# Kernel optimization log

Measured on AMD Instinct MI355X. Metric: run time of the kernel, lower is better.

## Reference

```python
import jax, jax.numpy as jnp
import numpy as np

DIM = 1024
H = 16
DH = DIM // H  # 64


def _l2norm(a):
    # matches torch F.normalize(dim=-1, eps=1e-12)
    n = jnp.linalg.norm(a, axis=-1, keepdims=True)
    return a / jnp.maximum(n, 1e-12)


def setup_inputs() -> dict:
    key = jax.random.key(0)
    ks = jax.random.split(key, 6)
    B, T = 4, 4096
    s = 0.02
    return {
        "x": jax.random.normal(ks[0], (B, T, DIM), jnp.float32),
        "Wqkv": jax.random.normal(ks[1], (3 * DIM, DIM), jnp.float32) * s,
        "Wg": jax.random.normal(ks[2], (H, DIM), jnp.float32) * s,
        "bg": jnp.zeros((H,), jnp.float32),
        "Wb": jax.random.normal(ks[3], (H, DIM), jnp.float32) * s,
        "bb": jnp.zeros((H,), jnp.float32),
        "Wout": jax.random.normal(ks[4], (DIM, DIM), jnp.float32) * s,
    }


def reference(x, Wqkv, Wg, bg, Wb, bb, Wout):
    B, T, D = x.shape
    qkv = (x @ Wqkv.T).reshape(B, T, 3, H, DH)
    q = _l2norm(qkv[:, :, 0])   # [B,T,H,Dh]
    k = _l2norm(qkv[:, :, 1])
    v = qkv[:, :, 2]
    alpha = jax.nn.sigmoid(x @ Wg.T + bg)  # [B,T,H]
    beta = jax.nn.sigmoid(x @ Wb.T + bb)   # [B,T,H]

    # time-major for scan
    qT = jnp.moveaxis(q, 1, 0)  # [T,B,H,Dh]
    kT = jnp.moveaxis(k, 1, 0)
    vT = jnp.moveaxis(v, 1, 0)
    aT = jnp.moveaxis(alpha, 1, 0)  # [T,B,H]
    bT = jnp.moveaxis(beta, 1, 0)

    S0 = jnp.zeros((B, H, DH, DH), jnp.float32)

    def step(S, inp):
        q_t, k_t, v_t, a_t, b_t = inp
        Sk = jnp.einsum('bhij,bhj->bhi', S, k_t)          # S @ k_t
        a = a_t[..., None, None]
        b = b_t[..., None, None]
        # S = a * (S - b * (S k) k^T) + b * v k^T
        S = a * (S - b * Sk[..., :, None] * k_t[..., None, :]) \
            + b * v_t[..., :, None] * k_t[..., None, :]
        o = jnp.einsum('bhij,bhj->bhi', S, q_t)
        return S, o

    _, outs = jax.lax.scan(step, S0, (qT, kT, vT, aT, bT))  # [T,B,H,Dh]
    out = jnp.moveaxis(outs, 0, 1).reshape(B, T, D)
    return out @ Wout.T
```

## Files before the change

### kernel.cpp

```cpp
#include <hip/hip_runtime.h>
#include <hip/hip_bf16.h>

#define NB   4
#define NT   4096
#define BT   16384
#define NDIM 1024
#define NH   16
#define NDH  64
#define CC   64
#define NCH  (NT / CC)
#define NPAIR 64
#define NU   (NPAIR * NCH)
#define DBS  24

using u16 = unsigned short;
typedef __bf16 bf16x8 __attribute__((ext_vector_type(8)));
typedef float f32x4 __attribute__((ext_vector_type(4)));
typedef unsigned short u16x8 __attribute__((ext_vector_type(8)));
typedef unsigned short u16x4 __attribute__((ext_vector_type(4)));

__device__ __forceinline__ float bf2f(u16 b) { return __uint_as_float(((unsigned)b) << 16); }
__device__ __forceinline__ u16 f2bf(float f) {
  return __builtin_bit_cast(u16, __float2bfloat16(f));
}
__device__ __forceinline__ int swz(int row, int e) { return e ^ ((row & 7) << 3); }
__device__ __forceinline__ bf16x8 zfrag() {
  u16x8 z = {0, 0, 0, 0, 0, 0, 0, 0};
  return __builtin_bit_cast(bf16x8, z);
}
__device__ __forceinline__ long qkvT_idx(int s, int h, long bt, int d) {
  return ((long)(s * 16 + h) * BT + bt) * 64 + d;
}

__global__ __launch_bounds__(256) void k_f32_to_bf16(const float* __restrict__ in,
                                                     u16* __restrict__ out, long n4) {
  long i = (long)blockIdx.x * blockDim.x + threadIdx.x;
  if (i >= n4) return;
  float4 f = reinterpret_cast<const float4*>(in)[i];
  u16x4 o;
  o.x = f2bf(f.x); o.y = f2bf(f.y); o.z = f2bf(f.z); o.w = f2bf(f.w);
  reinterpret_cast<u16x4*>(out)[i] = o;
}

__global__ __launch_bounds__(256) void k_build_wgb(const float* __restrict__ Wg,
                                                   const float* __restrict__ Wb,
                                                   u16* __restrict__ out) {
  int i = blockIdx.x * 256 + threadIdx.x;
  int row = i >> 10, col = i & 1023;
  float f = 0.f;
  if (row < 16)       f = Wg[row * 1024 + col];
  else if (row < 32)  f = Wb[(row - 16) * 1024 + col];
  out[i] = f2bf(f);
}

typedef unsigned int u32_as1 __attribute__((address_space(1)));
typedef unsigned int u32_as3 __attribute__((address_space(3)));
__device__ __forceinline__ void gload_lds16(const void* g, void* l) {
  __builtin_amdgcn_global_load_lds((const u32_as1*)g, (u32_as3*)l, 16, 0, 0);
}

template <typename OutT>
__global__ __launch_bounds__(256) void k_gemm_bt(const u16* __restrict__ A,
                                                 const u16* __restrict__ B,
                                                 OutT* __restrict__ C,
                                                 int M, int N, int K) {
  constexpr int BM = 128, BN = 128, BK = 32;
  __shared__ __align__(16) u16 As[BM * BK];
  __shared__ __align__(16) u16 Bs[BN * BK];
  const int tid = threadIdx.x;
  const int l = tid & 63, w = tid >> 6;
  const int tn = blockIdx.x, tm = blockIdx.y;
  const long a0 = (long)tm * BM * K;
  const long b0 = (long)tn * BN * K;
  const int srow = tid >> 2;
  const int scol = (tid & 3) << 3;
  const int wrow = (w >> 1) << 6;
  const int wcol = (w & 1) << 6;
  const int fr = l & 15, fq = l >> 4;

  f32x4 acc[4][4];
#pragma unroll
  for (int m = 0; m < 4; ++m)
#pragma unroll
    for (int n = 0; n < 4; ++n) acc[m][n] = f32x4{0.f, 0.f, 0.f, 0.f};

  for (int kk = 0; kk < K; kk += BK) {
    __syncthreads();
    const u16* gA = A + a0 + (long)srow * K + kk + scol;
    const u16* gB = B + b0 + (long)srow * K + kk + scol;
    gload_lds16(gA,                &As[(w * 16) * BK]);
    gload_lds16(gA + 64 * (long)K, &As[(64 + w * 16) * BK]);
    gload_lds16(gB,                &Bs[(w * 16) * BK]);
    gload_lds16(gB + 64 * (long)K, &Bs[(64 + w * 16) * BK]);
    __syncthreads();

    bf16x8 af[4], bfv[4];
#pragma unroll
    for (int m = 0; m < 4; ++m)
      af[m] = *(const bf16x8*)&As[(wrow + m * 16 + fr) * BK + (fq << 3)];
#pragma unroll
    for (int n = 0; n < 4; ++n)
      bfv[n] = *(const bf16x8*)&Bs[(wcol + n * 16 + fr) * BK + (fq << 3)];
#pragma unroll
    for (int m = 0; m < 4; ++m)
#pragma unroll
      for (int n = 0; n < 4; ++n)
        acc[m][n] = __builtin_amdgcn_mfma_f32_16x16x32_bf16(af[m], bfv[n], acc[m][n], 0, 0, 0);
  }

#pragma unroll
  for (int m = 0; m < 4; ++m) {
#pragma unroll
    for (int n = 0; n < 4; ++n) {
      const int r0 = tm * BM + wrow + m * 16 + fq * 4;
      const int c  = tn * BN + wcol + n * 16 + fr;
#pragma unroll
      for (int r = 0; r < 4; ++r) {
        float v = acc[m][n][r];
        long idx = (long)(r0 + r) * N + c;
        if constexpr (sizeof(OutT) == 2) C[idx] = f2bf(v);
        else                             C[idx] = v;
      }
    }
  }
}

template <typename OutT, bool QKVT>
__global__ __launch_bounds__(512, 2) void k_gemm256(const u16* __restrict__ A,
                                                    const u16* __restrict__ B,
                                                    OutT* __restrict__ C,
                                                    int M, int N, int K) {
  __shared__ __align__(16) u16 As[2][2][256 * 32];
  __shared__ __align__(16) u16 Bs[2][2][256 * 32];
  const int tid = threadIdx.x;
  const int l = tid & 63, w = tid >> 6;
  const int wm = w >> 2, wn = w & 3;
  const int fr = l & 15, fq = l >> 4;
  const int nwg = gridDim.x;
  const int cpx = nwg >> 3;
  const int bid = blockIdx.x;
  const int sbid = (bid & 7) * cpx + (bid >> 3);
  const int ntn = N >> 8;
  const int tm = sbid / ntn, tn = sbid - tm * ntn;
  const long a0 = (long)tm * 256 * K;
  const long b0 = (long)tn * 256 * K;
  const int srow0 = tid >> 2;
  const int scol8 = (((tid & 3) ^ ((tid >> 4) & 3)) << 3);
  const int cswz = ((fq ^ ((fr >> 2) & 3)) << 3);
  const int NKT = K >> 6;

  auto stage_half = [&](int kt, int buf, int hf) {
    const int ks = hf >> 1;
    const u16* Gp = (hf & 1) ? B : A;
    const long g0 = ((hf & 1) ? b0 : a0) + (long)kt * 64 + ks * 32 + scol8;
    u16* lb = (hf & 1) ? &Bs[buf][ks][w * 512] : &As[buf][ks][w * 512];
#pragma unroll
    for (int r = 0; r < 2; ++r)
      gload_lds16(Gp + g0 + (long)(r * 128 + srow0) * K, lb + r * 4096);
  };

  f32x4 acc[8][4];
#pragma unroll
  for (int m = 0; m < 8; ++m)
#pragma unroll
    for (int n = 0; n < 4; ++n) acc[m][n] = f32x4{0.f, 0.f, 0.f, 0.f};

  stage_half(0, 0, 0); stage_half(0, 0, 1); stage_half(0, 0, 2); stage_half(0, 0, 3);

  for (int kt = 0; kt < NKT; ++kt) {
    const int bi = kt & 1;
    const bool pf = (kt + 1 < NKT);
    asm volatile("s_waitcnt vmcnt(4)" ::: "memory");
    __builtin_amdgcn_sched_barrier(0);
    __builtin_amdgcn_s_barrier();
    __builtin_amdgcn_sched_barrier(0);
    {
      const u16* ap = &As[bi][0][(wm * 128 + fr) * 32 + cswz];
      const u16* bp = &Bs[bi][0][(wn * 64 + fr) * 32 + cswz];
      bf16x8 bfr[4], afr[4];
#pragma unroll
      for (int n = 0; n < 4; ++n) bfr[n] = *(const bf16x8*)(bp + n * 512);
#pragma unroll
      for (int m = 0; m < 4; ++m) afr[m] = *(const bf16x8*)(ap + m * 512);
      if (pf) stage_half(kt + 1, bi ^ 1, 0);
      __builtin_amdgcn_s_setprio(1);
#pragma unroll
      for (int m = 0; m < 4; ++m)
#pragma unroll
        for (int n = 0; n < 4; ++n)
          acc[m][n] = __builtin_amdgcn_mfma_f32_16x16x32_bf16(afr[m], bfr[n], acc[m][n], 0, 0, 0);
      __builtin_amdgcn_s_setprio(0);
#pragma unroll
      for (int m = 0; m < 4; ++m) afr[m] = *(const bf16x8*)(ap + (4 + m) * 512);
      if (pf) stage_half(kt + 1, bi ^ 1, 1);
      __builtin_amdgcn_s_setprio(1);
#pragma unroll
      for (int m = 0; m < 4; ++m)
#pragma unroll
        for (int n = 0; n < 4; ++n)
          acc[4 + m][n] = __builtin_amdgcn_mfma_f32_16x16x32_bf16(afr[m], bfr[n], acc[4 + m][n], 0, 0, 0);
      __builtin_amdgcn_s_setprio(0);
    }
    if (pf) { asm volatile("s_waitcnt vmcnt(4)" ::: "memory"); }
    else    { asm volatile("s_waitcnt vmcnt(0)" ::: "memory"); }
    __builtin_amdgcn_sched_barrier(0);
    __builtin_amdgcn_s_barrier();
    __builtin_amdgcn_sched_barrier(0);
    {
      const u16* ap = &As[bi][1][(wm * 128 + fr) * 32 + cswz];
      const u16* bp = &Bs[bi][1][(wn * 64 + fr) * 32 + cswz];
      bf16x8 bfr[4], afr[4];
#pragma unroll
      for (int n = 0; n < 4; ++n) bfr[n] = *(const bf16x8*)(bp + n * 512);
#pragma unroll
      for (int m = 0; m < 4; ++m) afr[m] = *(const bf16x8*)(ap + m * 512);
      if (pf) stage_half(kt + 1, bi ^ 1, 2);
      __builtin_amdgcn_s_setprio(1);
#pragma unroll
      for (int m = 0; m < 4; ++m)
#pragma unroll
        for (int n = 0; n < 4; ++n)
          acc[m][n] = __builtin_amdgcn_mfma_f32_16x16x32_bf16(afr[m], bfr[n], acc[m][n], 0, 0, 0);
      __builtin_amdgcn_s_setprio(0);
#pragma unroll
      for (int m = 0; m < 4; ++m) afr[m] = *(const bf16x8*)(ap + (4 + m) * 512);
      if (pf) stage_half(kt + 1, bi ^ 1, 3);
      __builtin_amdgcn_s_setprio(1);
#pragma unroll
      for (int m = 0; m < 4; ++m)
#pragma unroll
        for (int n = 0; n < 4; ++n)
          acc[4 + m][n] = __builtin_amdgcn_mfma_f32_16x16x32_bf16(afr[m], bfr[n], acc[4 + m][n], 0, 0, 0);
      __builtin_amdgcn_s_setprio(0);
    }
  }

#pragma unroll
  for (int m = 0; m < 8; ++m)
#pragma unroll
    for (int n = 0; n < 4; ++n) {
      const int row0 = tm * 256 + wm * 128 + m * 16 + fq * 4;
      const int col  = tn * 256 + wn * 64 + n * 16 + fr;
#pragma unroll
      for (int r = 0; r < 4; ++r) {
        if constexpr (QKVT) {
          const int hb = (tn * 256 + wn * 64) >> 6;
          long idx = ((long)hb * BT + (row0 + r)) * 64 + (n * 16 + fr);
          C[idx] = (OutT)f2bf(acc[m][n][r]);
        } else {
          long idx = (long)(row0 + r) * N + col;
          if constexpr (sizeof(OutT) == 2) C[idx] = f2bf(acc[m][n][r]);
          else                             C[idx] = acc[m][n][r];
        }
      }
    }
}

__global__ __launch_bounds__(256) void k_gates_fin(const float* __restrict__ raw,
                                                   const float* __restrict__ bg,
                                                   const float* __restrict__ bb,
                                                   float* __restrict__ alpha,
                                                   float* __restrict__ beta) {
  int i = blockIdx.x * 256 + threadIdx.x;
  if (i >= BT * NH) return;
  int bt = i >> 4, h = i & 15;
  float ga = raw[(long)bt * 128 + h] + bg[h];
  float gb = raw[(long)bt * 128 + 16 + h] + bb[h];
  alpha[i] = 1.f / (1.f + __expf(-ga));
  beta[i]  = 1.f / (1.f + __expf(-gb));
}

__global__ __launch_bounds__(256, 3) void k_prep(u16* __restrict__ qkv,
                                                 const float* __restrict__ alpha,
                                                 const float* __restrict__ beta,
                                                 float* __restrict__ A63G,
                                                 u16* __restrict__ oi) {
  __shared__ __align__(16) u16 Ks[64 * 64];
  __shared__ __align__(16) u16 WTs[128 * 64];
  __shared__ __align__(16) u16 Lb[64 * 64];
  __shared__ __align__(16) u16 MqS[64 * 64];
  __shared__ __align__(16) u16 KdT[64 * 64];
  __shared__ __align__(16) u16 Db[4 * 16 * DBS];
  __shared__ float cvec[64], Avec[64], bvec[64], nkinv[64], nqinv[64];

  const int unit = blockIdx.x;
  const int pair = unit >> 6, ch = unit & 63;
  const int b = pair >> 4, h = pair & 15;
  const int tid = threadIdx.x, l = tid & 63, w = tid >> 6;
  const int fr = l & 15, fq = l >> 4;
  const long t0 = (long)b * NT + (long)ch * CC;

  u16x8 kreg[2], vreg[2], qreg[2];
  int srow_[2], sseg_[2];
#pragma unroll
  for (int p = 0; p < 2; ++p) {
    int idx = p * 256 + tid;
    srow_[p] = idx >> 3; sseg_[p] = (idx & 7) * 8;
    qreg[p] = *(const u16x8*)&qkv[qkvT_idx(0, h, t0 + srow_[p], sseg_[p])];
    kreg[p] = *(const u16x8*)&qkv[qkvT_idx(1, h, t0 + srow_[p], sseg_[p])];
    vreg[p] = *(const u16x8*)&qkv[qkvT_idx(2, h, t0 + srow_[p], sseg_[p])];
  }
  const int ar = w * 16 + fr;
  u16x8 qa[2];
#pragma unroll
  for (int kk = 0; kk < 2; ++kk)
    qa[kk] = *(const u16x8*)&qkv[qkvT_idx(0, h, t0 + ar, kk * 32 + fq * 8)];

  if (w == 0) {
    float av = alpha[(t0 + l) * 16 + h];
    float bv = beta[(t0 + l) * 16 + h];
    float cl = __log2f(av);
#pragma unroll
    for (int d = 1; d < 64; d <<= 1) {
      float up = __shfl_up(cl, d);
      if (l >= d) cl += up;
    }
    float A = exp2f(cl);
    cvec[l] = cl; Avec[l] = A; bvec[l] = bv;
    if (l == 63) A63G[unit] = A;
  }
  __syncthreads();

#pragma unroll
  for (int p = 0; p < 2; ++p) {
    int row = srow_[p], seg = sseg_[p];
    *(u16x8*)&Ks[row * 64 + swz(row, seg)] = kreg[p];
    float kss = 0.f, qss = 0.f;
    const float bs = bvec[row];
#pragma unroll
    for (int e = 0; e < 8; ++e) {
      float kf = bf2f(kreg[p][e]), qf = bf2f(qreg[p][e]);
      kss += kf * kf; qss += qf * qf;
      int c = seg + e;
      WTs[c * 64 + swz(c, row)] = f2bf(bs * bf2f(vreg[p][e]));
    }
    kss += __shfl_xor(kss, 1); kss += __shfl_xor(kss, 2); kss += __shfl_xor(kss, 4);
    qss += __shfl_xor(qss, 1); qss += __shfl_xor(qss, 2); qss += __shfl_xor(qss, 4);
    if ((tid & 7) == 0) { nkinv[row] = kss; nqinv[row] = qss; }
  }
  __syncthreads();

  if (tid < 64)       nkinv[tid] = rsqrtf(fmaxf(nkinv[tid], 1e-24f));
  else if (tid < 128) nqinv[tid - 64] = rsqrtf(fmaxf(nqinv[tid - 64], 1e-24f));
  __syncthreads();

  f32x4 akk[4], aqk[4];
#pragma unroll
  for (int n = 0; n < 4; ++n) { akk[n] = f32x4{0, 0, 0, 0}; aqk[n] = f32x4{0, 0, 0, 0}; }
  {
    bf16x8 afK[2], afQ[2];
#pragma unroll
    for (int kk = 0; kk < 2; ++kk) {
      afK[kk] = __builtin_bit_cast(bf16x8, *(const u16x8*)&Ks[ar * 64 + swz(ar, kk * 32 + fq * 8)]);
      afQ[kk] = __builtin_bit_cast(bf16x8, qa[kk]);
    }
#pragma unroll
    for (int n = 0; n < 4; ++n) {
      const int br = n * 16 + fr;
#pragma unroll
      for (int kk = 0; kk < 2; ++kk) {
        bf16x8 bk = __builtin_bit_cast(bf16x8, *(const u16x8*)&Ks[br * 64 + swz(br, kk * 32 + fq * 8)]);
        akk[n] = __builtin_amdgcn_mfma_f32_16x16x32_bf16(afK[kk], bk, akk[n], 0, 0, 0);
        aqk[n] = __builtin_amdgcn_mfma_f32_16x16x32_bf16(afQ[kk], bk, aqk[n], 0, 0, 0);
      }
    }
  }
  {
    const int j = tid & 63, tg4 = tid >> 6;
    const float c63 = cvec[63];
    u16 kb[16], kd[16];
#pragma unroll
    for (int tt = 0; tt < 16; ++tt) {
      int t = tg4 * 16 + tt;
      float kv = bf2f(Ks[t * 64 + swz(t, j)]) * nkinv[t];
      kb[tt] = f2bf(bvec[t] * Avec[t] * kv);
      kd[tt] = f2bf(exp2f(c63 - cvec[t]) * kv);
    }
#pragma unroll
    for (int g8 = 0; g8 < 2; ++g8) {
      u16x8 o1, o2;
#pragma unroll
      for (int e = 0; e < 8; ++e) { o1[e] = kb[g8 * 8 + e]; o2[e] = kd[g8 * 8 + e]; }
      int colg = tg4 * 16 + g8 * 8;
      *(u16x8*)&WTs[(64 + j) * 64 + swz(64 + j, colg)] = o1;
      *(u16x8*)&KdT[j * 64 + swz(j, colg)] = o2;
    }
  }
#pragma unroll
  for (int n = 0; n < 4; ++n)
#pragma unroll
    for (int r = 0; r < 4; ++r) {
      const int t = w * 16 + fq * 4 + r;
      const int s = n * 16 + fr;
      const float e = exp2f(cvec[t] - cvec[s]);
      Lb[t * 64 + swz(t, s)] = (s < t) ? f2bf(bvec[t] * e * nkinv[t] * nkinv[s] * akk[n][r]) : (u16)0;
      MqS[t * 64 + swz(t, s)] = (s <= t) ? f2bf(e * nqinv[t] * nkinv[s] * aqk[n][r]) : (u16)0;
    }
  __syncthreads();

  if (l < 16) {
    const int c = l;
    const int rb = w * 16;
    float x[16];
#pragma unroll
    for (int u = 0; u < 16; ++u) {
      float a2 = (u == c) ? 1.f : 0.f;
#pragma unroll
      for (int s = 0; s < u; ++s)
        a2 -= bf2f(Lb[(rb + u) * 64 + swz(rb + u, rb + s)]) * x[s];
      x[u] = a2;
    }
#pragma unroll
    for (int u = 0; u < 16; ++u)
      Db[w * 16 * DBS + u * DBS + c] = f2bf(x[u]);
  }
  __syncthreads();

  float ltil[6];
  {
    const int pbi[6] = {1, 2, 2, 3, 3, 3}, pbj[6] = {0, 0, 1, 0, 1, 2};
    const int tt = tid >> 4, s = tid & 15;
#pragma unroll
    for (int e = 0; e < 6; ++e) {
      int bi = pbi[e], bj = pbj[e];
      float a2 = 0.f;
#pragma unroll
      for (int u = 0; u < 16; ++u)
        a2 += bf2f(Db[bi * 16 * DBS + tt * DBS + u]) *
              bf2f(Lb[(bi * 16 + u) * 64 + swz(bi * 16 + u, bj * 16 + s)]);
      ltil[e] = a2;
    }
  }
  f32x4 rtacc[2][4];
#pragma unroll
  for (int rt2 = 0; rt2 < 2; ++rt2) {
    const int rrow = (w * 2 + rt2) * 16 + fr;
#pragma unroll
    for (int bi = 0; bi < 4; ++bi) {
      bf16x8 a2 = (fq < 2)
        ? __builtin_bit_cast(bf16x8, *(const u16x8*)&WTs[rrow * 64 + swz(rrow, bi * 16 + fq * 8)])
        : zfrag();
      bf16x8 b2 = (fq < 2)
        ? __builtin_bit_cast(bf16x8, *(const u16x8*)&Db[bi * 16 * DBS + fr * DBS + fq * 8])
        : zfrag();
      rtacc[rt2][bi] = __builtin_amdgcn_mfma_f32_16x16x32_bf16(a2, b2, f32x4{0, 0, 0, 0}, 0, 0, 0);
    }
  }
  __syncthreads();
  {
    const int pbi[6] = {1, 2, 2, 3, 3, 3}, pbj[6] = {0, 0, 1, 0, 1, 2};
    const int tt = tid >> 4, s = tid & 15;
#pragma unroll
    for (int e = 0; e < 6; ++e)
      Lb[(pbi[e] * 16 + tt) * 64 + swz(pbi[e] * 16 + tt, pbj[e] * 16 + s)] = f2bf(-ltil[e]);
  }
#pragma unroll
  for (int rt2 = 0; rt2 < 2; ++rt2)
#pragma unroll
    for (int bi = 0; bi < 4; ++bi)
#pragma unroll
      for (int r = 0; r < 4; ++r) {
        int rr = (w * 2 + rt2) * 16 + fq * 4 + r;
        WTs[rr * 64 + swz(rr, bi * 16 + fr)] = f2bf(rtacc[rt2][bi][r]);
      }
  __syncthreads();

#pragma unroll
  for (int rt2 = 0; rt2 < 2; ++rt2) {
    const int rrow = (w * 2 + rt2) * 16 + fr;
    const int wr0 = (w * 2 + rt2) * 16 + fq * 4;
#pragma unroll
    for (int i = 1; i < 4; ++i) {
      f32x4 a2;
#pragma unroll
      for (int r = 0; r < 4; ++r)
        a2[r] = bf2f(WTs[(wr0 + r) * 64 + swz(wr0 + r, i * 16 + fr)]);
      {
        bf16x8 af = __builtin_bit_cast(bf16x8, *(const u16x8*)&WTs[rrow * 64 + swz(rrow, fq * 8)]);
        bf16x8 bf_;
        if (i == 1) bf_ = (fq < 2)
          ? __builtin_bit_cast(bf16x8, *(const u16x8*)&Lb[(16 + fr) * 64 + swz(16 + fr, fq * 8)])
          : zfrag();
        else bf_ = __builtin_bit_cast(bf16x8, *(const u16x8*)&Lb[(i * 16 + fr) * 64 + swz(i * 16 + fr, fq * 8)]);
        a2 = __builtin_amdgcn_mfma_f32_16x16x32_bf16(af, bf_, a2, 0, 0, 0);
      }
      if (i == 3) {
        bf16x8 af = __builtin_bit_cast(bf16x8, *(const u16x8*)&WTs[rrow * 64 + swz(rrow, 32 + fq * 8)]);
        bf16x8 bf_ = (fq < 2)
          ? __builtin_bit_cast(bf16x8, *(const u16x8*)&Lb[(48 + fr) * 64 + swz(48 + fr, 32 + fq * 8)])
          : zfrag();
        a2 = __builtin_amdgcn_mfma_f32_16x16x32_bf16(af, bf_, a2, 0, 0, 0);
      }
#pragma unroll
      for (int r = 0; r < 4; ++r)
        WTs[(wr0 + r) * 64 + swz(wr0 + r, i * 16 + fr)] = f2bf(a2[r]);
    }
  }
  __syncthreads();

  u16 qpre[4][4];
#pragma unroll
  for (int n = 0; n < 4; ++n)
#pragma unroll
    for (int r = 0; r < 4; ++r)
      qpre[n][r] = qkv[qkvT_idx(0, h, t0 + w * 16 + fq * 4 + r, n * 16 + fr)];

  f32x4 aG[4], aU[4], aQe[4], aOi[4];
#pragma unroll
  for (int n = 0; n < 4; ++n) {
    aG[n] = f32x4{0, 0, 0, 0}; aU[n] = f32x4{0, 0, 0, 0};
    aQe[n] = f32x4{0, 0, 0, 0}; aOi[n] = f32x4{0, 0, 0, 0};
  }
  {
    bf16x8 aKd[2], aWv[2], aMq[2];
#pragma unroll
    for (int kk = 0; kk < 2; ++kk) {
      aKd[kk] = __builtin_bit_cast(bf16x8, *(const u16x8*)&KdT[ar * 64 + swz(ar, kk * 32 + fq * 8)]);
      aWv[kk] = __builtin_bit_cast(bf16x8, *(const u16x8*)&WTs[ar * 64 + swz(ar, kk * 32 + fq * 8)]);
      aMq[kk] = __builtin_bit_cast(bf16x8, *(const u16x8*)&MqS[ar * 64 + swz(ar, kk * 32 + fq * 8)]);
    }
#pragma unroll
    for (int n = 0; n < 4; ++n) {
      const int br = n * 16 + fr;
#pragma unroll
      for (int kk = 0; kk < 2; ++kk) {
        bf16x8 bTw = __builtin_bit_cast(bf16x8, *(const u16x8*)&WTs[(64 + br) * 64 + swz(64 + br, kk * 32 + fq * 8)]);
        bf16x8 bKd = __builtin_bit_cast(bf16x8, *(const u16x8*)&KdT[br * 64 + swz(br, kk * 32 + fq * 8)]);
        bf16x8 bWv = __builtin_bit_cast(bf16x8, *(const u16x8*)&WTs[br * 64 + swz(br, kk * 32 + fq * 8)]);
        aG[n]  = __builtin_amdgcn_mfma_f32_16x16x32_bf16(aKd[kk], bTw, aG[n], 0, 0, 0);
        aU[n]  = __builtin_amdgcn_mfma_f32_16x16x32_bf16(aWv[kk], bKd, aU[n], 0, 0, 0);
        aQe[n] = __builtin_amdgcn_mfma_f32_16x16x32_bf16(aMq[kk], bTw, aQe[n], 0, 0, 0);
        aOi[n] = __builtin_amdgcn_mfma_f32_16x16x32_bf16(aMq[kk], bWv, aOi[n], 0, 0, 0);
      }
    }
  }
  asm volatile("s_waitcnt vmcnt(0)" ::: "memory");
  __builtin_amdgcn_sched_barrier(0);
#pragma unroll
  for (int n = 0; n < 4; ++n)
#pragma unroll
    for (int r = 0; r < 4; ++r) {
      const int i = w * 16 + fq * 4 + r;
      const int cn = n * 16 + fr;
      const int sw = swz(i, cn);
      qkv[qkvT_idx(0, h, t0 + i, sw)] = f2bf(Avec[i] * nqinv[i] * bf2f(qpre[n][r]) - aQe[n][r]);
      qkv[qkvT_idx(1, h, t0 + i, sw)] = f2bf(-aG[n][r]);
      qkv[qkvT_idx(2, h, t0 + i, sw)] = f2bf(aU[n][r]);
      Ks[i * 64 + cn] = f2bf(aOi[n][r]);
    }
  __syncthreads();
#pragma unroll
  for (int p = 0; p < 2; ++p) {
    const int idx = p * 256 + tid;
    const int row = idx >> 3, seg = (idx & 7) * 8;
    *(u16x8*)&oi[(long)unit * 4096 + row * 64 + seg] = *(const u16x8*)&Ks[row * 64 + seg];
  }
}

__global__ __launch_bounds__(256) void k_seq(const u16* __restrict__ qkv,
                                             const u16* __restrict__ oi,
                                             const float* __restrict__ A63G,
                                             u16* __restrict__ ob) {
  __shared__ __align__(16) u16 Sb[64 * 64];
  __shared__ __align__(16) u16 Obs[64 * 64];
  __shared__ __align__(16) u16 stg[2][4][64 * 64];
  __shared__ float a63s[64];
  const int pair = blockIdx.x;
  const int b = pair >> 4, h = pair & 15;
  const int tid = threadIdx.x, l = tid & 63, w = tid >> 6;
  const int fr = l & 15, fq = l >> 4;
  const int ar = w * 16 + fr;

  auto stage = [&](int c, int bi) {
    const long tg = (long)b * NT + (long)c * CC;
#pragma unroll
    for (int m = 0; m < 4; ++m)
#pragma unroll
      for (int p = 0; p < 2; ++p) {
        int idx = p * 256 + tid;
        int row = idx >> 3, seg = (idx & 7) * 8;
        const u16* src = (m < 3)
          ? &qkv[qkvT_idx(m, h, tg + row, seg)]
          : &oi[(long)(pair * 64 + c) * 4096 + row * 64 + seg];
        gload_lds16(src, &stg[bi][m][p * 2048 + w * 512]);
      }
  };

  if (tid < 64) a63s[tid] = A63G[pair * 64 + tid];
  for (int i = tid; i < 4096; i += 256) Sb[i] = 0;
  stage(0, 0);
  f32x4 sacc[4];
#pragma unroll
  for (int n = 0; n < 4; ++n) sacc[n] = f32x4{0, 0, 0, 0};
  asm volatile("s_waitcnt lgkmcnt(0)" ::: "memory");
  __builtin_amdgcn_sched_barrier(0);

  for (int c = 0; c < NCH; ++c) {
    const int bi = c & 1;
    const long tg = (long)b * NT + (long)c * CC;
    if (c + 1 < NCH) {
      stage(c + 1, bi ^ 1);
      asm volatile("s_waitcnt vmcnt(8)" ::: "memory");
    } else {
      asm volatile("s_waitcnt vmcnt(0)" ::: "memory");
    }
    __builtin_amdgcn_sched_barrier(0);
    __builtin_amdgcn_s_barrier();
    __builtin_amdgcn_sched_barrier(0);

    const u16* Qe = stg[bi][0];
    const u16* Gm = stg[bi][1];
    const u16* Um = stg[bi][2];
    const u16* Obl = stg[bi][3];

    bf16x8 aq[2];
#pragma unroll
    for (int kk = 0; kk < 2; ++kk)
      aq[kk] = __builtin_bit_cast(bf16x8, *(const u16x8*)&Qe[ar * 64 + swz(ar, kk * 32 + fq * 8)]);
    f32x4 ao[4];
#pragma unroll
    for (int n = 0; n < 4; ++n) ao[n] = f32x4{0, 0, 0, 0};
#pragma unroll
    for (int n = 0; n < 4; ++n) {
      const int br = n * 16 + fr;
#pragma unroll
      for (int kk = 0; kk < 2; ++kk) {
        bf16x8 sb = __builtin_bit_cast(bf16x8, *(const u16x8*)&Sb[br * 64 + swz(br, kk * 32 + fq * 8)]);
        ao[n] = __builtin_amdgcn_mfma_f32_16x16x32_bf16(aq[kk], sb, ao[n], 0, 0, 0);
      }
    }
    bf16x8 as_[2];
#pragma unroll
    for (int kk = 0; kk < 2; ++kk)
      as_[kk] = __builtin_bit_cast(bf16x8, *(const u16x8*)&Sb[ar * 64 + swz(ar, kk * 32 + fq * 8)]);
    const float A63 = a63s[c];
#pragma unroll
    for (int n = 0; n < 4; ++n) {
#pragma unroll
      for (int r = 0; r < 4; ++r) sacc[n][r] *= A63;
      const int br = n * 16 + fr;
#pragma unroll
      for (int kk = 0; kk < 2; ++kk) {
        bf16x8 g = __builtin_bit_cast(bf16x8, *(const u16x8*)&Gm[br * 64 + swz(br, kk * 32 + fq * 8)]);
        sacc[n] = __builtin_amdgcn_mfma_f32_16x16x32_bf16(as_[kk], g, sacc[n], 0, 0, 0);
      }
    }
#pragma unroll
    for (int n = 0; n < 4; ++n)
#pragma unroll
      for (int r = 0; r < 4; ++r) {
        const int i = w * 16 + fq * 4 + r;
        const int cn = n * 16 + fr;
        sacc[n][r] += bf2f(Um[i * 64 + swz(i, cn)]);
        Obs[i * 64 + cn] = f2bf(bf2f(Obl[i * 64 + cn]) + ao[n][r]);
      }
    asm volatile("s_waitcnt lgkmcnt(0)" ::: "memory");
    __builtin_amdgcn_s_barrier();
#pragma unroll
    for (int n = 0; n < 4; ++n)
#pragma unroll
      for (int r = 0; r < 4; ++r) {
        const int d = w * 16 + fq * 4 + r, j = n * 16 + fr;
        Sb[d * 64 + swz(d, j)] = f2bf(sacc[n][r]);
      }
#pragma unroll
    for (int p = 0; p < 2; ++p) {
      const int idx = p * 256 + tid;
      const int row = idx >> 3, seg = (idx & 7) * 8;
      *(u16x8*)&ob[(tg + row) * 1024 + h * 64 + seg] = *(const u16x8*)&Obs[row * 64 + seg];
    }
    asm volatile("s_waitcnt lgkmcnt(0)" ::: "memory");
    __builtin_amdgcn_sched_barrier(0);
  }
}

extern "C" void kernel_launch(void* const* d_in, const int* in_sizes, int n_in,
                              void* d_out, int out_size, void* d_ws, size_t ws_size,
                              hipStream_t stream) {
  const float* x    = (const float*)d_in[0];
  const float* Wqkv = (const float*)d_in[1];
  const float* Wg   = (const float*)d_in[2];
  const float* bg   = (const float*)d_in[3];
  const float* Wb   = (const float*)d_in[4];
  const float* bb   = (const float*)d_in[5];
  const float* Wout = (const float*)d_in[6];
  float* out = (float*)d_out;

  char* ws = (char*)d_ws;
  u16* xb    = (u16*)ws;
  u16* wqkvb = xb    + (long)BT * NDIM;
  u16* woutb = wqkvb + (long)3072 * 1024;
  u16* wgbb  = woutb + (long)1024 * 1024;
  u16* qkvb  = wgbb  + (long)128 * 1024;
  u16* ob    = qkvb  + (long)BT * 3072;
  float* graw  = (float*)(ob + (long)BT * NDIM);
  float* alpha = graw + (long)BT * 128;
  float* beta  = alpha + (long)BT * NH;
  float* A63G  = graw;
  u16*   oi    = xb;

  k_f32_to_bf16<<<(BT * (long)NDIM / 4 + 255) / 256, 256, 0, stream>>>(x, xb, BT * (long)NDIM / 4);
  k_f32_to_bf16<<<(3072L * 1024 / 4 + 255) / 256, 256, 0, stream>>>(Wqkv, wqkvb, 3072L * 1024 / 4);
  k_f32_to_bf16<<<(1024L * 1024 / 4 + 255) / 256, 256, 0, stream>>>(Wout, woutb, 1024L * 1024 / 4);
  k_build_wgb<<<(128 * 1024) / 256, 256, 0, stream>>>(Wg, Wb, wgbb);

  k_gemm256<u16, true><<<64 * 12, 512, 0, stream>>>(xb, wqkvb, qkvb, BT, 3072, NDIM);

  k_gemm_bt<float><<<dim3(1, BT / 128), 256, 0, stream>>>(xb, wgbb, graw, BT, 128, NDIM);
  k_gates_fin<<<(BT * NH + 255) / 256, 256, 0, stream>>>(graw, bg, bb, alpha, beta);

  k_prep<<<NU, 256, 0, stream>>>(qkvb, alpha, beta, A63G, oi);
  k_seq<<<NPAIR, 256, 0, stream>>>(qkvb, oi, A63G, ob);

  k_gemm256<float, false><<<64 * 4, 512, 0, stream>>>(ob, woutb, out, BT, NDIM, NDIM);
}
```

Before: 411.8 us.

## Split sequential chunk kernel across 16 waves, one 16x16 tile each

The per-(batch,head) sequential state-update kernel now launches 1024 threads instead of 256, so each of 16 waves computes one 16x16 output/state tile instead of each of 4 waves computing a 16x64 strip. This shortens the per-chunk critical path of the serial recurrence, which runs on only 64 blocks. Staging loads are restricted to the first 512 threads and the vmcnt wait is adjusted to match. The cost is more barrier participants and more redundant LDS fragment loads.

```diff
diff --git a/kernel.cpp b/kernel.cpp
--- a/kernel.cpp
+++ b/kernel.cpp
@@ -557,10 +557,10 @@
   }
 }
 
-__global__ __launch_bounds__(256) void k_seq(const u16* __restrict__ qkv,
-                                             const u16* __restrict__ oi,
-                                             const float* __restrict__ A63G,
-                                             u16* __restrict__ ob) {
+__global__ __launch_bounds__(1024) void k_seq(const u16* __restrict__ qkv,
+                                              const u16* __restrict__ oi,
+                                              const float* __restrict__ A63G,
+                                              u16* __restrict__ ob) {
   __shared__ __align__(16) u16 Sb[64 * 64];
   __shared__ __align__(16) u16 Obs[64 * 64];
   __shared__ __align__(16) u16 stg[2][4][64 * 64];
@@ -569,29 +569,26 @@
   const int b = pair >> 4, h = pair & 15;
   const int tid = threadIdx.x, l = tid & 63, w = tid >> 6;
   const int fr = l & 15, fq = l >> 4;
-  const int ar = w * 16 + fr;
+  const int tw = w >> 2, td = w & 3;
 
   auto stage = [&](int c, int bi) {
     const long tg = (long)b * NT + (long)c * CC;
-#pragma unroll
-    for (int m = 0; m < 4; ++m)
-#pragma unroll
-      for (int p = 0; p < 2; ++p) {
-        int idx = p * 256 + tid;
-        int row = idx >> 3, seg = (idx & 7) * 8;
+    if (tid < 512) {
+      const int row = tid >> 3, seg = (tid & 7) * 8;
+#pragma unroll
+      for (int m = 0; m < 4; ++m) {
         const u16* src = (m < 3)
           ? &qkv[qkvT_idx(m, h, tg + row, seg)]
           : &oi[(long)(pair * 64 + c) * 4096 + row * 64 + seg];
-        gload_lds16(src, &stg[bi][m][p * 2048 + w * 512]);
-      }
+        gload_lds16(src, &stg[bi][m][row * 64 + seg]);
+      }
+    }
   };
 
   if (tid < 64) a63s[tid] = A63G[pair * 64 + tid];
-  for (int i = tid; i < 4096; i += 256) Sb[i] = 0;
+  for (int i = tid; i < 4096; i += 1024) Sb[i] = 0;
   stage(0, 0);
-  f32x4 sacc[4];
-#pragma unroll
-  for (int n = 0; n < 4; ++n) sacc[n] = f32x4{0, 0, 0, 0};
+  f32x4 sacc = f32x4{0, 0, 0, 0};
   asm volatile("s_waitcnt lgkmcnt(0)" ::: "memory");
   __builtin_amdgcn_sched_barrier(0);
 
@@ -600,7 +597,7 @@
     const long tg = (long)b * NT + (long)c * CC;
     if (c + 1 < NCH) {
       stage(c + 1, bi ^ 1);
-      asm volatile("s_waitcnt vmcnt(8)" ::: "memory");
+      asm volatile("s_waitcnt vmcnt(4)" ::: "memory");
     } else {
       asm volatile("s_waitcnt vmcnt(0)" ::: "memory");
     }
@@ -613,60 +610,37 @@
     const u16* Um = stg[bi][2];
     const u16* Obl = stg[bi][3];
 
-    bf16x8 aq[2];
-#pragma unroll
-    for (int kk = 0; kk < 2; ++kk)
-      aq[kk] = __builtin_bit_cast(bf16x8, *(const u16x8*)&Qe[ar * 64 + swz(ar, kk * 32 + fq * 8)]);
-    f32x4 ao[4];
-#pragma unroll
-    for (int n = 0; n < 4; ++n) ao[n] = f32x4{0, 0, 0, 0};
-#pragma unroll
-    for (int n = 0; n < 4; ++n) {
-      const int br = n * 16 + fr;
-#pragma unroll
-      for (int kk = 0; kk < 2; ++kk) {
-        bf16x8 sb = __builtin_bit_cast(bf16x8, *(const u16x8*)&Sb[br * 64 + swz(br, kk * 32 + fq * 8)]);
-        ao[n] = __builtin_amdgcn_mfma_f32_16x16x32_bf16(aq[kk], sb, ao[n], 0, 0, 0);
-      }
-    }
-    bf16x8 as_[2];
-#pragma unroll
-    for (int kk = 0; kk < 2; ++kk)
-      as_[kk] = __builtin_bit_cast(bf16x8, *(const u16x8*)&Sb[ar * 64 + swz(ar, kk * 32 + fq * 8)]);
+    const int at = tw * 16 + fr;
+    const int bd = td * 16 + fr;
+    f32x4 ao = f32x4{0, 0, 0, 0};
     const float A63 = a63s[c];
 #pragma unroll
-    for (int n = 0; n < 4; ++n) {
-#pragma unroll
-      for (int r = 0; r < 4; ++r) sacc[n][r] *= A63;
-      const int br = n * 16 + fr;
-#pragma unroll
-      for (int kk = 0; kk < 2; ++kk) {
-        bf16x8 g = __builtin_bit_cast(bf16x8, *(const u16x8*)&Gm[br * 64 + swz(br, kk * 32 + fq * 8)]);
-        sacc[n] = __builtin_amdgcn_mfma_f32_16x16x32_bf16(as_[kk], g, sacc[n], 0, 0, 0);
-      }
-    }
-#pragma unroll
-    for (int n = 0; n < 4; ++n)
-#pragma unroll
-      for (int r = 0; r < 4; ++r) {
-        const int i = w * 16 + fq * 4 + r;
-        const int cn = n * 16 + fr;
-        sacc[n][r] += bf2f(Um[i * 64 + swz(i, cn)]);
-        Obs[i * 64 + cn] = f2bf(bf2f(Obl[i * 64 + cn]) + ao[n][r]);
-      }
+    for (int r = 0; r < 4; ++r) sacc[r] *= A63;
+#pragma unroll
+    for (int kk = 0; kk < 2; ++kk) {
+      bf16x8 aq = __builtin_bit_cast(bf16x8, *(const u16x8*)&Qe[at * 64 + swz(at, kk * 32 + fq * 8)]);
+      bf16x8 sb = __builtin_bit_cast(bf16x8, *(const u16x8*)&Sb[bd * 64 + swz(bd, kk * 32 + fq * 8)]);
+      ao = __builtin_amdgcn_mfma_f32_16x16x32_bf16(aq, sb, ao, 0, 0, 0);
+      bf16x8 as_ = __builtin_bit_cast(bf16x8, *(const u16x8*)&Sb[at * 64 + swz(at, kk * 32 + fq * 8)]);
+      bf16x8 g  = __builtin_bit_cast(bf16x8, *(const u16x8*)&Gm[bd * 64 + swz(bd, kk * 32 + fq * 8)]);
+      sacc = __builtin_amdgcn_mfma_f32_16x16x32_bf16(as_, g, sacc, 0, 0, 0);
+    }
+#pragma unroll
+    for (int r = 0; r < 4; ++r) {
+      const int ri = tw * 16 + fq * 4 + r;
+      const int cj = td * 16 + fr;
+      sacc[r] += bf2f(Um[ri * 64 + swz(ri, cj)]);
+      Obs[ri * 64 + cj] = f2bf(bf2f(Obl[ri * 64 + cj]) + ao[r]);
+    }
     asm volatile("s_waitcnt lgkmcnt(0)" ::: "memory");
     __builtin_amdgcn_s_barrier();
 #pragma unroll
-    for (int n = 0; n < 4; ++n)
-#pragma unroll
-      for (int r = 0; r < 4; ++r) {
-        const int d = w * 16 + fq * 4 + r, j = n * 16 + fr;
-        Sb[d * 64 + swz(d, j)] = f2bf(sacc[n][r]);
-      }
-#pragma unroll
-    for (int p = 0; p < 2; ++p) {
-      const int idx = p * 256 + tid;
-      const int row = idx >> 3, seg = (idx & 7) * 8;
+    for (int r = 0; r < 4; ++r) {
+      const int d = tw * 16 + fq * 4 + r, j = td * 16 + fr;
+      Sb[d * 64 + swz(d, j)] = f2bf(sacc[r]);
+    }
+    if (tid < 512) {
+      const int row = tid >> 3, seg = (tid & 7) * 8;
       *(u16x8*)&ob[(tg + row) * 1024 + h * 64 + seg] = *(const u16x8*)&Obs[row * 64 + seg];
     }
     asm volatile("s_waitcnt lgkmcnt(0)" ::: "memory");
@@ -710,7 +684,7 @@
   k_gates_fin<<<(BT * NH + 255) / 256, 256, 0, stream>>>(graw, bg, bb, alpha, beta);
 
   k_prep<<<NU, 256, 0, stream>>>(qkvb, alpha, beta, A63G, oi);
-  k_seq<<<NPAIR, 256, 0, stream>>>(qkvb, oi, A63G, ob);
+  k_seq<<<NPAIR, 1024, 0, stream>>>(qkvb, oi, A63G, ob);
 
   k_gemm256<float, false><<<64 * 4, 512, 0, stream>>>(ob, woutb, out, BT, NDIM, NDIM);
 }
```

Measured after the change: 388.4 us. 5.7% less time.
